# Performance work log

Measured on AMD Instinct MI355X. Metric: run time of the kernel, lower is better.

The kernel has to match this reference:

```python
import jax, jax.numpy as jnp
import numpy as np
from jax import lax

IMG = 28
K = 3
OUT = IMG - K + 1  # 26

def setup_inputs() -> dict:
    key = jax.random.key(0)
    k1, k2, k3 = jax.random.split(key, 3)
    B = 32768
    x = jax.random.normal(k1, (B, IMG * IMG), dtype=jnp.float32)
    conv_w = jax.random.normal(k2, (K, K), dtype=jnp.float32)
    W = jax.random.normal(k3, (IMG * IMG - 0, 1), dtype=jnp.float32)  # placeholder
    W = jax.random.normal(k3, (OUT * OUT, 10), dtype=jnp.float32) * 0.02
    b = jnp.zeros((10,), dtype=jnp.float32)
    return {"x": x, "conv_w": conv_w, "W": W, "b": b}

def reference(x, conv_w, W, b):
    B = x.shape[0]
    img = x.reshape(B, 1, IMG, IMG)            # NCHW
    ker = conv_w.reshape(1, 1, K, K)           # OIHW
    # The original Convolve is cross-correlation (slice * weight), which
    # matches lax.conv_general_dilated's default semantics.
    conv = lax.conv_general_dilated(
        img, ker, window_strides=(1, 1), padding='VALID',
        dimension_numbers=('NCHW', 'OIHW', 'NCHW'))  # [B,1,26,26]
    h = jax.nn.relu(conv.reshape(B, OUT * OUT))
    return h @ W + b
```

## Files before the change

kernel.cpp:

```cpp
#include <hip/hip_runtime.h>

#define IMGD 28
#define OUTD 26
#define NCLS 10
#define NIMG 64
#define UPB 29
#define BWORDS (NIMG * UPB * 4)
#define NBAND 7
#define THREADS 1024
#define LDSTRIDE 11

typedef float v2f __attribute__((ext_vector_type(2)));

__device__ __forceinline__ void gload_lds16(const float* gp, float* lp) {
    __builtin_amdgcn_global_load_lds(
        (const __attribute__((address_space(1))) void*)gp,
        (__attribute__((address_space(3))) void*)lp, 16, 0, 0);
}

__device__ __forceinline__ void stage_band(const float* __restrict__ x,
                                           int img_base, int B, int r0,
                                           float* buf, int wv, int lane)
{
#pragma unroll
    for (int it = 0; it < 2; ++it) {
        const int fw = it * 16 + wv;
        if (fw < UPB) {
            const int f = fw * 64 + lane;
            const int g = f / UPB;
            const int s = f - g * UPB;
            const int q = (s == 28) ? 27 : s;
            int gi = img_base + g; if (gi >= B) gi = B - 1;
            const float* gp = x + (size_t)gi * (IMGD * IMGD) + r0 * IMGD + q * 4;
            gload_lds16(gp, buf + fw * 256);
        }
    }
}

template<int NU>
__device__ __forceinline__ void read_row(const float* buf, int lane, int br, int u0,
                                         float* dst)
{
    const float4* b4 = (const float4*)buf;
#pragma unroll
    for (int u = 0; u < NU; ++u) {
        float4 a = b4[lane * UPB + br * 7 + u0 + u];
        dst[4*u+0] = a.x; dst[4*u+1] = a.y; dst[4*u+2] = a.z; dst[4*u+3] = a.w;
    }
}

template<int WID, int OFF>
__device__ __forceinline__ void conv_row(const float* X, const float* Y, const float* Z,
                                         const float (&kk)[9],
                                         const float* __restrict__ wr, v2f* acc)
{
#pragma unroll
    for (int c = 0; c < WID; ++c) {
        float p0 = fmaf(X[OFF+c], kk[0], X[OFF+c+1] * kk[1]);
        p0 = fmaf(X[OFF+c+2], kk[2], p0);
        float p1 = fmaf(Y[OFF+c], kk[3], Y[OFF+c+1] * kk[4]);
        p1 = fmaf(Y[OFF+c+2], kk[5], p1);
        float p2 = fmaf(Z[OFF+c], kk[6], Z[OFF+c+1] * kk[7]);
        p2 = fmaf(Z[OFF+c+2], kk[8], p2);
        float v = fmaxf((p0 + p1) + p2, 0.0f);
        const float* w = wr + c * NCLS;
#pragma unroll
        for (int p = 0; p < 5; ++p) {
            v2f wv2 = *(const v2f*)(w + 2 * p);
            v2f vv; vv[0] = v; vv[1] = v;
            acc[p] += vv * wv2;
        }
    }
}

template<int WID, int NU, int OFF>
__device__ __forceinline__ void run_all(
    const float* __restrict__ x, int img_base, int B,
    float* lds0, int wv, int lane, int rg, int u0, int c0,
    const float* __restrict__ cw, const float* __restrict__ Wp, v2f* acc)
{
    float kk[9];
#pragma unroll
    for (int i = 0; i < 9; ++i) kk[i] = cw[i];

    float S[2][4 * NU];

    stage_band(x, img_base, B, 0, lds0,          wv, lane);
    stage_band(x, img_base, B, 4, lds0 + BWORDS, wv, lane);

    for (int k = 0; k < NBAND; ++k) {
        if (k < NBAND - 1) {
            if (wv < 13) asm volatile("s_waitcnt vmcnt(2)" ::: "memory");
            else         asm volatile("s_waitcnt vmcnt(1)" ::: "memory");
        } else {
            asm volatile("s_waitcnt vmcnt(0)" ::: "memory");
        }
        __builtin_amdgcn_s_barrier();

        const float* buf = lds0 + (k & 1) * BWORDS;

        if (rg == 0) {
            float R[4][4 * NU];
#pragma unroll
            for (int br = 0; br < 4; ++br) read_row<NU>(buf, lane, br, u0, R[br]);
            conv_row<WID, OFF>(R[0], R[1], R[2], kk,
                               Wp + ((size_t)(4 * k) * OUTD + c0) * NCLS, acc);
            conv_row<WID, OFF>(R[1], R[2], R[3], kk,
                               Wp + ((size_t)(4 * k + 1) * OUTD + c0) * NCLS, acc);
        } else {
            if (k > 0) {
                float T[2][4 * NU];
                read_row<NU>(buf, lane, 0, u0, T[0]);
                read_row<NU>(buf, lane, 1, u0, T[1]);
                conv_row<WID, OFF>(S[0], S[1], T[0], kk,
                                   Wp + ((size_t)(4 * k - 2) * OUTD + c0) * NCLS, acc);
                conv_row<WID, OFF>(S[1], T[0], T[1], kk,
                                   Wp + ((size_t)(4 * k - 1) * OUTD + c0) * NCLS, acc);
            }
            if (k < NBAND - 1) {
                read_row<NU>(buf, lane, 2, u0, S[0]);
                read_row<NU>(buf, lane, 3, u0, S[1]);
            }
        }

        asm volatile("" ::: "memory");
        __builtin_amdgcn_s_barrier();
        asm volatile("" ::: "memory");

        if (k + 2 < NBAND)
            stage_band(x, img_base, B, 4 * (k + 2), lds0 + (k & 1) * BWORDS, wv, lane);
    }
}

__global__ __launch_bounds__(THREADS, 8) void fused_conv_relu_fc(
    const float* __restrict__ x,
    const float* __restrict__ cw,
    const float* __restrict__ Wp,
    const float* __restrict__ bp,
    float* __restrict__ out,
    int B)
{
    __shared__ float lds[2 * BWORDS];

    const int lane = threadIdx.x & 63;
    const int wv   = __builtin_amdgcn_readfirstlane((int)(threadIdx.x >> 6));
    const int rg   = wv >> 3;
    const int cs   = wv & 7;
    const int img_base = blockIdx.x * NIMG;

    v2f acc[5];
#pragma unroll
    for (int p = 0; p < 5; ++p) { acc[p][0] = 0.0f; acc[p][1] = 0.0f; }

    if      (cs < 5)  run_all<4,2,0>(x, img_base, B, lds, wv, lane, rg, cs, 4*cs, cw, Wp, acc);
    else if (cs == 5) run_all<2,1,0>(x, img_base, B, lds, wv, lane, rg, 5,  20,   cw, Wp, acc);
    else if (cs == 6) run_all<2,2,2>(x, img_base, B, lds, wv, lane, rg, 5,  22,   cw, Wp, acc);
    else              run_all<2,1,0>(x, img_base, B, lds, wv, lane, rg, 6,  24,   cw, Wp, acc);

    __syncthreads();

    float* part = lds;
    float* myp = &part[(wv * 64 + lane) * LDSTRIDE];
#pragma unroll
    for (int p = 0; p < 5; ++p) { myp[2*p] = acc[p][0]; myp[2*p+1] = acc[p][1]; }
    __syncthreads();

    const int o = threadIdx.x;
    if (o < NIMG * NCLS) {
        const int im = o / NCLS;
        const int c  = o - im * NCLS;
        float s = bp[c];
#pragma unroll
        for (int w2 = 0; w2 < 16; ++w2)
            s += part[(w2 * 64 + im) * LDSTRIDE + c];
        if (img_base + im < B)
            out[(size_t)(img_base + im) * NCLS + c] = s;
    }
}

extern "C" void kernel_launch(void* const* d_in, const int* in_sizes, int n_in,
                              void* d_out, int out_size, void* d_ws, size_t ws_size,
                              hipStream_t stream) {
    const float* x  = (const float*)d_in[0];
    const float* cw = (const float*)d_in[1];
    const float* Wp = (const float*)d_in[2];
    const float* bp = (const float*)d_in[3];
    float* out = (float*)d_out;

    const int B = in_sizes[0] / (IMGD * IMGD);
    const int grid = (B + NIMG - 1) / NIMG;

    fused_conv_relu_fc<<<grid, THREADS, 0, stream>>>(x, cw, Wp, bp, out, B);
}
```

Before: 32.55 us.

## Stage five input rows per band instead of four to cut band iterations

Each double-buffered LDS band now holds 5 input rows (35 float4 units per image) instead of 4 with padding. The loop drops from 7 bands to 6, with a 3-row tail band. Row group 0 computes 3 output rows per band and row group 1 computes 2, reusing the rows it carried over. This removes one barrier/stage round and the wasted duplicate padding unit, at the cost of a larger LDS footprint (which may lower occupancy) and more complex vmcnt accounting.

```diff
diff --git a/kernel.cpp b/kernel.cpp
--- a/kernel.cpp
+++ b/kernel.cpp
@@ -4,9 +4,10 @@
 #define OUTD 26
 #define NCLS 10
 #define NIMG 64
-#define UPB 29
+#define UPB 35
+#define UPB_T 21
 #define BWORDS (NIMG * UPB * 4)
-#define NBAND 7
+#define NBAND 6
 #define THREADS 1024
 #define LDSTRIDE 11
 
@@ -18,33 +19,33 @@
         (__attribute__((address_space(3))) void*)lp, 16, 0, 0);
 }
 
+template<int UNITS>
 __device__ __forceinline__ void stage_band(const float* __restrict__ x,
                                            int img_base, int B, int r0,
                                            float* buf, int wv, int lane)
 {
 #pragma unroll
-    for (int it = 0; it < 2; ++it) {
+    for (int it = 0; it < 3; ++it) {
         const int fw = it * 16 + wv;
-        if (fw < UPB) {
+        if (fw < UNITS) {
             const int f = fw * 64 + lane;
-            const int g = f / UPB;
-            const int s = f - g * UPB;
-            const int q = (s == 28) ? 27 : s;
+            const int g = f / UNITS;
+            const int s = f - g * UNITS;
             int gi = img_base + g; if (gi >= B) gi = B - 1;
-            const float* gp = x + (size_t)gi * (IMGD * IMGD) + r0 * IMGD + q * 4;
+            const float* gp = x + (size_t)gi * (IMGD * IMGD) + r0 * IMGD + s * 4;
             gload_lds16(gp, buf + fw * 256);
         }
     }
 }
 
-template<int NU>
+template<int NU, int STRIDE>
 __device__ __forceinline__ void read_row(const float* buf, int lane, int br, int u0,
                                          float* dst)
 {
     const float4* b4 = (const float4*)buf;
 #pragma unroll
     for (int u = 0; u < NU; ++u) {
-        float4 a = b4[lane * UPB + br * 7 + u0 + u];
+        float4 a = b4[lane * STRIDE + br * 7 + u0 + u];
         dst[4*u+0] = a.x; dst[4*u+1] = a.y; dst[4*u+2] = a.z; dst[4*u+3] = a.w;
     }
 }
@@ -83,52 +84,79 @@
 #pragma unroll
     for (int i = 0; i < 9; ++i) kk[i] = cw[i];
 
-    float S[2][4 * NU];
-
-    stage_band(x, img_base, B, 0, lds0,          wv, lane);
-    stage_band(x, img_base, B, 4, lds0 + BWORDS, wv, lane);
-
-    for (int k = 0; k < NBAND; ++k) {
-        if (k < NBAND - 1) {
-            if (wv < 13) asm volatile("s_waitcnt vmcnt(2)" ::: "memory");
-            else         asm volatile("s_waitcnt vmcnt(1)" ::: "memory");
+    float S0[4 * NU], S1[4 * NU];
+
+    stage_band<UPB>(x, img_base, B, 0, lds0,          wv, lane);
+    stage_band<UPB>(x, img_base, B, 5, lds0 + BWORDS, wv, lane);
+
+    for (int k = 0; k < NBAND - 1; ++k) {
+        if (k == NBAND - 2) {
+            if (wv < 5) asm volatile("s_waitcnt vmcnt(2)" ::: "memory");
+            else        asm volatile("s_waitcnt vmcnt(1)" ::: "memory");
         } else {
-            asm volatile("s_waitcnt vmcnt(0)" ::: "memory");
+            if (wv < 3) asm volatile("s_waitcnt vmcnt(3)" ::: "memory");
+            else        asm volatile("s_waitcnt vmcnt(2)" ::: "memory");
         }
         __builtin_amdgcn_s_barrier();
 
         const float* buf = lds0 + (k & 1) * BWORDS;
 
         if (rg == 0) {
-            float R[4][4 * NU];
-#pragma unroll
-            for (int br = 0; br < 4; ++br) read_row<NU>(buf, lane, br, u0, R[br]);
-            conv_row<WID, OFF>(R[0], R[1], R[2], kk,
-                               Wp + ((size_t)(4 * k) * OUTD + c0) * NCLS, acc);
-            conv_row<WID, OFF>(R[1], R[2], R[3], kk,
-                               Wp + ((size_t)(4 * k + 1) * OUTD + c0) * NCLS, acc);
+            float Ra[4*NU], Rb[4*NU], Rc[4*NU], Rd[4*NU], Re[4*NU];
+            read_row<NU, UPB>(buf, lane, 0, u0, Ra);
+            read_row<NU, UPB>(buf, lane, 1, u0, Rb);
+            read_row<NU, UPB>(buf, lane, 2, u0, Rc);
+            conv_row<WID, OFF>(Ra, Rb, Rc, kk,
+                               Wp + ((size_t)(5 * k) * OUTD + c0) * NCLS, acc);
+            read_row<NU, UPB>(buf, lane, 3, u0, Rd);
+            conv_row<WID, OFF>(Rb, Rc, Rd, kk,
+                               Wp + ((size_t)(5 * k + 1) * OUTD + c0) * NCLS, acc);
+            read_row<NU, UPB>(buf, lane, 4, u0, Re);
+            conv_row<WID, OFF>(Rc, Rd, Re, kk,
+                               Wp + ((size_t)(5 * k + 2) * OUTD + c0) * NCLS, acc);
         } else {
             if (k > 0) {
-                float T[2][4 * NU];
-                read_row<NU>(buf, lane, 0, u0, T[0]);
-                read_row<NU>(buf, lane, 1, u0, T[1]);
-                conv_row<WID, OFF>(S[0], S[1], T[0], kk,
-                                   Wp + ((size_t)(4 * k - 2) * OUTD + c0) * NCLS, acc);
-                conv_row<WID, OFF>(S[1], T[0], T[1], kk,
-                                   Wp + ((size_t)(4 * k - 1) * OUTD + c0) * NCLS, acc);
+                float Ta[4*NU], Tb[4*NU];
+                read_row<NU, UPB>(buf, lane, 0, u0, Ta);
+                read_row<NU, UPB>(buf, lane, 1, u0, Tb);
+                conv_row<WID, OFF>(S0, S1, Ta, kk,
+                                   Wp + ((size_t)(5 * k - 2) * OUTD + c0) * NCLS, acc);
+                conv_row<WID, OFF>(S1, Ta, Tb, kk,
+                                   Wp + ((size_t)(5 * k - 1) * OUTD + c0) * NCLS, acc);
             }
-            if (k < NBAND - 1) {
-                read_row<NU>(buf, lane, 2, u0, S[0]);
-                read_row<NU>(buf, lane, 3, u0, S[1]);
-            }
-        }
-
-        asm volatile("" ::: "memory");
-        __builtin_amdgcn_s_barrier();
-        asm volatile("" ::: "memory");
-
-        if (k + 2 < NBAND)
-            stage_band(x, img_base, B, 4 * (k + 2), lds0 + (k & 1) * BWORDS, wv, lane);
+            read_row<NU, UPB>(buf, lane, 3, u0, S0);
+            read_row<NU, UPB>(buf, lane, 4, u0, S1);
+        }
+
+        if (k <= NBAND - 3) {
+            asm volatile("" ::: "memory");
+            __builtin_amdgcn_s_barrier();
+            asm volatile("" ::: "memory");
+            if (k == 3)
+                stage_band<UPB_T>(x, img_base, B, 25, lds0 + (k & 1) * BWORDS, wv, lane);
+            else
+                stage_band<UPB>(x, img_base, B, 5 * (k + 2), lds0 + (k & 1) * BWORDS, wv, lane);
+        }
+    }
+
+    asm volatile("s_waitcnt vmcnt(0)" ::: "memory");
+    __builtin_amdgcn_s_barrier();
+    const float* buf = lds0 + BWORDS;
+    if (rg == 0) {
+        float Ta[4*NU], Tb[4*NU], Tc[4*NU];
+        read_row<NU, UPB_T>(buf, lane, 0, u0, Ta);
+        read_row<NU, UPB_T>(buf, lane, 1, u0, Tb);
+        read_row<NU, UPB_T>(buf, lane, 2, u0, Tc);
+        conv_row<WID, OFF>(Ta, Tb, Tc, kk,
+                           Wp + ((size_t)25 * OUTD + c0) * NCLS, acc);
+    } else {
+        float Ta[4*NU], Tb[4*NU];
+        read_row<NU, UPB_T>(buf, lane, 0, u0, Ta);
+        read_row<NU, UPB_T>(buf, lane, 1, u0, Tb);
+        conv_row<WID, OFF>(S0, S1, Ta, kk,
+                           Wp + ((size_t)23 * OUTD + c0) * NCLS, acc);
+        conv_row<WID, OFF>(S1, Ta, Tb, kk,
+                           Wp + ((size_t)24 * OUTD + c0) * NCLS, acc);
     }
 }
 
```

Measured after the change: 32.71 us, median of 4. About the same (+0.5%).
